# Kernel optimization log

Hardware: AMD Instinct MI355X
Metric: run time of the kernel (lower is better)

## Reference

```python
import jax, jax.numpy as jnp
import numpy as np
from jax import lax

LATENT_DIM = 512
TOKEN_DIM = 256
KERNEL = 5
STRIDE = 5


def setup_inputs() -> dict:
    key = jax.random.key(0)
    ks = jax.random.split(key, 8)
    B, L, S = 8, 1024, 10240
    s = lambda fan_in: 1.0 / np.sqrt(fan_in)
    return {
        "latents": jax.random.normal(ks[0], (B, L, LATENT_DIM), dtype=jnp.float32),
        "tokens": jax.random.normal(ks[1], (B, S, TOKEN_DIM), dtype=jnp.float32),
        # nn.Linear weights, stored as (out, in) like torch
        "W_lat": jax.random.uniform(ks[2], (LATENT_DIM, LATENT_DIM), jnp.float32, -s(LATENT_DIM), s(LATENT_DIM)),
        "W_tok": jax.random.uniform(ks[3], (LATENT_DIM, LATENT_DIM), jnp.float32, -s(LATENT_DIM), s(LATENT_DIM)),
        "W_vlat": jax.random.uniform(ks[4], (LATENT_DIM, LATENT_DIM), jnp.float32, -s(LATENT_DIM), s(LATENT_DIM)),
        "W_vtok": jax.random.uniform(ks[5], (LATENT_DIM, LATENT_DIM), jnp.float32, -s(LATENT_DIM), s(LATENT_DIM)),
        # Conv1d weight (out_ch, in_ch, k) and bias
        "conv_w": jax.random.uniform(ks[6], (LATENT_DIM, TOKEN_DIM, KERNEL), jnp.float32, -s(TOKEN_DIM * KERNEL), s(TOKEN_DIM * KERNEL)),
        "conv_b": jax.random.uniform(ks[7], (LATENT_DIM,), jnp.float32, -s(TOKEN_DIM * KERNEL), s(TOKEN_DIM * KERNEL)),
    }


def reference(latents, tokens, W_lat, W_tok, W_vlat, W_vtok, conv_w, conv_b):
    # Conv1d: (B,S,token_dim) -> (B,S//5,latent_dim)
    tok = lax.conv_general_dilated(
        tokens.transpose(0, 2, 1), conv_w, window_strides=(STRIDE,),
        padding="VALID", dimension_numbers=("NCH", "OIH", "NCH"))
    tok = (tok + conv_b[None, :, None]).transpose(0, 2, 1)  # (B, S', D)

    R_lat = jnp.einsum("bld,ed->ble", latents, W_lat)
    R_tok = jnp.einsum("bsd,ed->bse", tok, W_tok)
    V_lat = jnp.einsum("bld,ed->ble", latents, W_vlat)
    V_tok = jnp.einsum("bsd,ed->bse", tok, W_vtok)

    # shared score matrix, used for both row-wise and column-wise softmax
    A = jnp.einsum("ble,bse->bls", R_lat, R_tok) / jnp.sqrt(jnp.float32(LATENT_DIM))
    delta_lat = jnp.einsum("bls,bse->ble", jax.nn.softmax(A, axis=-1), V_tok)
    delta_tok = jnp.einsum("bls,ble->bse", jax.nn.softmax(A, axis=1), V_lat)

    updated_latents = latents + delta_lat
    updated_tokens = tok + delta_tok
    output = jnp.concatenate([updated_latents, updated_tokens], axis=1)
    return (updated_latents, updated_tokens, output)
```

## Files before the change

### kernel.cpp

```cpp
#include <hip/hip_runtime.h>
#include <math.h>

#define SCALEF 0.044194173824159216f

typedef __attribute__((ext_vector_type(8))) short bf16x8;
typedef __attribute__((ext_vector_type(4))) float f32x4;

static __device__ __forceinline__ unsigned short f2bf(float f) {
    union { float f; unsigned int i; } v; v.f = f;
    return (unsigned short)((v.i + 0x7fffu + ((v.i >> 16) & 1u)) >> 16);
}
static __device__ __forceinline__ float bf2f(unsigned short h) {
    union { unsigned int i; float f; } v; v.i = ((unsigned int)h) << 16;
    return v.f;
}
static __device__ __forceinline__ void gload16(const void* g, void* l) {
    __builtin_amdgcn_global_load_lds(
        (const __attribute__((address_space(1))) unsigned int*)g,
        (__attribute__((address_space(3))) unsigned int*)l, 16, 0, 0);
}

__global__ __launch_bounds__(256) void cvt_tl(const float4* __restrict__ tok,
                                              const float4* __restrict__ lat,
                                              ushort4* __restrict__ tokd,
                                              ushort4* __restrict__ latd) {
    long t = blockIdx.x * 256L + threadIdx.x;
    #pragma unroll
    for (int k = 0; k < 5; ++k) {
        long i = t + k * 1048576L;
        float4 f = tok[i];
        ushort4 u; u.x = f2bf(f.x); u.y = f2bf(f.y); u.z = f2bf(f.z); u.w = f2bf(f.w);
        tokd[i] = u;
    }
    {
        float4 f = lat[t];
        ushort4 u; u.x = f2bf(f.x); u.y = f2bf(f.y); u.z = f2bf(f.z); u.w = f2bf(f.w);
        latd[t] = u;
    }
}

__global__ __launch_bounds__(256) void prep_rest(
    const float4* __restrict__ wl, const float4* __restrict__ wt,
    const float4* __restrict__ wvl, const float4* __restrict__ wvt,
    const float* __restrict__ cw,
    ushort4* __restrict__ wlb, ushort4* __restrict__ wtb,
    ushort4* __restrict__ wvlb, ushort4* __restrict__ wvtb,
    unsigned int* __restrict__ wpb)
{
    const long NW = 65536, NCV = 327680;
    for (long i = blockIdx.x * 256L + threadIdx.x; i < 4 * NW + NCV;
         i += gridDim.x * 256L) {
        long r = i;
        const float4* s = nullptr; ushort4* d = nullptr;
        if (r < NW) { s = wl; d = wlb; }
        else if ((r -= NW) < NW) { s = wt; d = wtb; }
        else if ((r -= NW) < NW) { s = wvl; d = wvlb; }
        else if ((r -= NW) < NW) { s = wvt; d = wvtb; }
        else {
            r -= NW;
            long e = r / 640, rr = r % 640, k = rr >> 7, c2 = rr & 127;
            unsigned int lo = f2bf(cw[e * 1280 + (2 * c2) * 5 + k]);
            unsigned int hi = f2bf(cw[e * 1280 + (2 * c2 + 1) * 5 + k]);
            wpb[r] = lo | (hi << 16);
            continue;
        }
        float4 f = s[r];
        ushort4 u; u.x = f2bf(f.x); u.y = f2bf(f.y); u.z = f2bf(f.z); u.w = f2bf(f.w);
        d[r] = u;
    }
}

__global__ __launch_bounds__(256) void transpose_bf(const unsigned short* __restrict__ S,
                                                    unsigned short* __restrict__ ST) {
    __shared__ unsigned short tl[64][66];
    const int b = blockIdx.z, r0 = blockIdx.y << 6, c0 = blockIdx.x << 6;
    const unsigned short* Sb = S + ((long)b << 21);
    unsigned short* Tb = ST + ((long)b << 21);
    const int t32 = threadIdx.x & 31, trow = threadIdx.x >> 5;
    #pragma unroll
    for (int i = 0; i < 8; ++i) {
        int r = trow + i * 8;
        unsigned int v = *(const unsigned int*)&Sb[(long)(r0 + r) * 2048 + c0 + t32 * 2];
        *(unsigned int*)&tl[r][t32 * 2] = v;
    }
    __syncthreads();
    #pragma unroll
    for (int i = 0; i < 8; ++i) {
        int c = trow + i * 8;
        unsigned int lo = tl[t32 * 2][c], hi = tl[t32 * 2 + 1][c];
        *(unsigned int*)&Tb[(long)(c0 + c) * 1024 + r0 + t32 * 2] = lo | (hi << 16);
    }
}

template<int RL>
static __device__ __forceinline__ void sm_body(unsigned short* __restrict__ rowp,
                                               float* __restrict__ redm,
                                               float* __restrict__ reds) {
    constexpr int U = RL / 512;
    unsigned int* p = (unsigned int*)rowp;
    const int t = threadIdx.x, lane = t & 63, wid = t >> 6;
    unsigned int u[U];
    float v[2 * U];
    #pragma unroll
    for (int i = 0; i < U; ++i) u[i] = p[t + (i << 8)];
    #pragma unroll
    for (int i = 0; i < U; ++i) {
        v[2 * i]     = bf2f((unsigned short)(u[i] & 0xffffu));
        v[2 * i + 1] = bf2f((unsigned short)(u[i] >> 16));
    }
    float m = -INFINITY;
    #pragma unroll
    for (int i = 0; i < 2 * U; ++i) m = fmaxf(m, v[i]);
    #pragma unroll
    for (int k = 1; k < 64; k <<= 1) m = fmaxf(m, __shfl_xor(m, k));
    if (lane == 0) redm[wid] = m;
    __syncthreads();
    m = fmaxf(fmaxf(redm[0], redm[1]), fmaxf(redm[2], redm[3]));
    float s = 0.f, e[2 * U];
    #pragma unroll
    for (int i = 0; i < 2 * U; ++i) { e[i] = __expf(v[i] - m); s += e[i]; }
    #pragma unroll
    for (int k = 1; k < 64; k <<= 1) s += __shfl_xor(s, k);
    if (lane == 0) reds[wid] = s;
    __syncthreads();
    s = reds[0] + reds[1] + reds[2] + reds[3];
    float inv = 1.f / s;
    #pragma unroll
    for (int i = 0; i < U; ++i) {
        unsigned int lo = f2bf(e[2 * i] * inv);
        unsigned int hi = f2bf(e[2 * i + 1] * inv);
        p[t + (i << 8)] = lo | (hi << 16);
    }
}

__global__ __launch_bounds__(256) void softmax_both(unsigned short* __restrict__ S,
                                                    unsigned short* __restrict__ ST) {
    __shared__ float redm[4], reds[4];
    long b = blockIdx.x;
    if (b < 8192) sm_body<2048>(S + b * 2048L, redm, reds);
    else          sm_body<1024>(ST + (b - 8192) * 1024L, redm, reds);
}

template<int AMODE, int EPI>
static __device__ __forceinline__ void mm_body(
    char* __restrict__ smc, int bx, int by, int z,
    const unsigned short* __restrict__ A, const unsigned short* __restrict__ B,
    long bsA, long bsB, int lda, int ldb, int K,
    unsigned short* __restrict__ Cb, long bsCb,
    float* __restrict__ C0, long bsC0, float* __restrict__ C1, long bsC1,
    const void* __restrict__ basep, long bsBase, int ldc, float scale)
{
    const int t = threadIdx.x, lane = t & 63, wid = t >> 6;
    const int m0 = by << 7, n0 = bx << 7;
    const unsigned short* Ab = A + (long)z * bsA;
    const unsigned short* Bb = B + (long)z * bsB;

    const int rA0 = wid * 16 + (lane >> 2);
    const int rA1 = rA0 + 64;
    const int cs0 = (lane & 3) ^ ((rA0 >> 1) & 3);
    const int cs1 = (lane & 3) ^ ((rA1 >> 1) & 3);

    long aoff0, aoff1;
    if (AMODE == 0) {
        aoff0 = (long)(m0 + rA0) * lda + cs0 * 8;
        aoff1 = (long)(m0 + rA1) * lda + cs1 * 8;
    } else {
        int ma = m0 + rA0, mb = m0 + rA1;
        aoff0 = (long)(ma >> 11) * 2621440 + (long)(ma & 2047) * 1280 + cs0 * 8;
        aoff1 = (long)(mb >> 11) * 2621440 + (long)(mb & 2047) * 1280 + cs1 * 8;
    }
    const long boff0 = (long)(n0 + rA0) * ldb + cs0 * 8;
    const long boff1 = (long)(n0 + rA1) * ldb + cs1 * 8;

    const int dA0 = (wid << 10), dA1 = ((wid + 4) << 10);
    const int dB0 = 8192 + (wid << 10), dB1 = 8192 + ((wid + 4) << 10);

    const int wr = wid >> 1, wc = wid & 1;
    const int l15 = lane & 15, cslot = lane >> 4;
    int offA[4], offB[4];
    #pragma unroll
    for (int i = 0; i < 4; ++i) {
        int r = wr * 64 + i * 16 + l15;
        offA[i] = r * 64 + ((cslot ^ ((r >> 1) & 3)) << 4);
        int rb = wc * 64 + i * 16 + l15;
        offB[i] = 8192 + rb * 64 + ((cslot ^ ((rb >> 1) & 3)) << 4);
    }

    f32x4 acc[4][4];
    #pragma unroll
    for (int i = 0; i < 4; ++i)
        #pragma unroll
        for (int j = 0; j < 4; ++j)
            acc[i][j] = (f32x4)(0.f);

#define STAGE(p, ktv) do {                                   \
        int kb_ = (ktv);                                     \
        int bo_ = (p) * 16384;                               \
        gload16(Ab + aoff0 + kb_, smc + bo_ + dA0);          \
        gload16(Ab + aoff1 + kb_, smc + bo_ + dA1);          \
        gload16(Bb + boff0 + kb_, smc + bo_ + dB0);          \
        gload16(Bb + boff1 + kb_, smc + bo_ + dB1);          \
    } while (0)

    const int nt = K >> 5;
    STAGE(0, 0);
    STAGE(1, 32);
    int cur = 0;
    for (int it = 0; it < nt; ++it) {
        if (it + 2 < nt) {
            int nx2 = (cur >= 1) ? cur - 1 : 2;
            STAGE(nx2, (it + 2) << 5);
            asm volatile("s_waitcnt vmcnt(8)" ::: "memory");
        } else if (it + 1 < nt) {
            asm volatile("s_waitcnt vmcnt(4)" ::: "memory");
        } else {
            asm volatile("s_waitcnt vmcnt(0)" ::: "memory");
        }
        __builtin_amdgcn_s_barrier();
        const char* base = smc + cur * 16384;
        bf16x8 af[4], bfr[4];
        #pragma unroll
        for (int i = 0; i < 4; ++i) af[i]  = *(const bf16x8*)(base + offA[i]);
        #pragma unroll
        for (int i = 0; i < 4; ++i) bfr[i] = *(const bf16x8*)(base + offB[i]);
        #pragma unroll
        for (int i = 0; i < 4; ++i)
            #pragma unroll
            for (int j = 0; j < 4; ++j)
                acc[i][j] = __builtin_amdgcn_mfma_f32_16x16x32_bf16(af[i], bfr[j], acc[i][j], 0, 0, 0);
        asm volatile("s_waitcnt lgkmcnt(0)" ::: "memory");
        __builtin_amdgcn_s_barrier();
        cur = (cur + 1 == 3) ? 0 : cur + 1;
    }
#undef STAGE

    const int colb = n0 + wc * 64 + l15;
    const int rowb = m0 + wr * 64 + cslot * 4;
    #pragma unroll
    for (int i = 0; i < 4; ++i) {
        #pragma unroll
        for (int j = 0; j < 4; ++j) {
            int n = colb + j * 16;
            #pragma unroll
            for (int q = 0; q < 4; ++q) {
                int m = rowb + i * 16 + q;
                float v = acc[i][j][q];
                if (EPI == 0) {
                    Cb[(long)z * bsCb + (long)m * ldc + n] = f2bf(v * scale);
                } else if (EPI == 1) {
                    v += ((const float*)basep)[n];
                    Cb[(long)m * ldc + n] = f2bf(v);
                } else if (EPI == 2) {
                    float bv = ((const float*)basep)[(long)z * bsBase + (long)m * ldc + n];
                    float o = bv + v;
                    C0[(long)z * bsC0 + (long)m * ldc + n] = o;
                    C1[(long)z * bsC1 + (long)m * ldc + n] = o;
                } else {
                    float bv = bf2f(((const unsigned short*)basep)[(long)z * bsBase + (long)m * ldc + n]);
                    float o = bv + v;
                    C0[(long)z * bsC0 + (long)m * ldc + n] = o;
                    C1[(long)z * bsC1 + (long)m * ldc + n] = o;
                }
            }
        }
    }
}

template<int AMODE, int EPI>
__global__ __launch_bounds__(256) void mm_nt(
    const unsigned short* __restrict__ A, const unsigned short* __restrict__ B,
    long bsA, long bsB, int lda, int ldb, int K,
    unsigned short* __restrict__ Cb, long bsCb,
    float* __restrict__ C0, long bsC0, float* __restrict__ C1, long bsC1,
    const void* __restrict__ basep, long bsBase, int ldc, float scale)
{
    __shared__ unsigned short sm[24576];
    mm_body<AMODE, EPI>((char*)sm, blockIdx.x, blockIdx.y, blockIdx.z,
                        A, B, bsA, bsB, lda, ldb, K, Cb, bsCb,
                        C0, bsC0, C1, bsC1, basep, bsBase, ldc, scale);
}

__global__ __launch_bounds__(256) void gemm_g1(
    const unsigned short* __restrict__ tknb, const unsigned short* __restrict__ wpb,
    const float* __restrict__ conv_b, unsigned short* __restrict__ tokb,
    const unsigned short* __restrict__ latb, const unsigned short* __restrict__ wlb,
    unsigned short* __restrict__ rlat,
    const unsigned short* __restrict__ wvlb, unsigned short* __restrict__ vlT)
{
    __shared__ unsigned short sm[24576];
    char* smc = (char*)sm;
    const int bid = blockIdx.x;
    if (bid < 512) {
        int l = bid;
        mm_body<1, 1>(smc, l & 3, l >> 2, 0, tknb, wpb, 0, 0, 1280, 1280, 1280,
                      tokb, 0, nullptr, 0, nullptr, 0, conv_b, 0, 512, 1.f);
    } else if (bid < 768) {
        int l = bid - 512;
        mm_body<0, 0>(smc, l & 3, l >> 2, 0, latb, wlb, 0, 0, 512, 512, 512,
                      rlat, 0, nullptr, 0, nullptr, 0, nullptr, 0, 512, 1.f);
    } else {
        int l = bid - 768;
        mm_body<0, 0>(smc, l & 7, (l >> 3) & 3, l >> 5, wvlb, latb, 0, 524288,
                      512, 512, 512, vlT, 524288, nullptr, 0, nullptr, 0,
                      nullptr, 0, 1024, 1.f);
    }
}

__global__ __launch_bounds__(256) void gemm_g2(
    const unsigned short* __restrict__ tokb, const unsigned short* __restrict__ wtb,
    unsigned short* __restrict__ rtok,
    const unsigned short* __restrict__ wvtb, unsigned short* __restrict__ vtT)
{
    __shared__ unsigned short sm[24576];
    char* smc = (char*)sm;
    const int bid = blockIdx.x;
    if (bid < 512) {
        int l = bid;
        mm_body<0, 0>(smc, l & 3, l >> 2, 0, tokb, wtb, 0, 0, 512, 512, 512,
                      rtok, 0, nullptr, 0, nullptr, 0, nullptr, 0, 512, 1.f);
    } else {
        int l = bid - 512;
        mm_body<0, 0>(smc, l & 15, (l >> 4) & 3, l >> 6, wvtb, tokb, 0, 1048576,
                      512, 512, 512, vtT, 1048576, nullptr, 0, nullptr, 0,
                      nullptr, 0, 2048, 1.f);
    }
}

__global__ __launch_bounds__(256) void gemm_g3(
    const unsigned short* __restrict__ S, const unsigned short* __restrict__ ST,
    const unsigned short* __restrict__ vlT, const unsigned short* __restrict__ vtT,
    const float* __restrict__ latents, const unsigned short* __restrict__ tokb,
    float* __restrict__ out)
{
    __shared__ unsigned short sm[24576];
    char* smc = (char*)sm;
    const int bid = blockIdx.x;
    if (bid < 256) {
        int l = bid;
        mm_body<0, 2>(smc, l & 3, (l >> 2) & 7, l >> 5, S, vtT, 2097152, 1048576,
                      2048, 2048, 2048, nullptr, 0,
                      out, 524288, out + 12582912, 1572864,
                      latents, 524288, 512, 1.f);
    } else {
        int l = bid - 256;
        mm_body<0, 3>(smc, l & 3, (l >> 2) & 15, l >> 6, ST, vlT, 2097152, 524288,
                      1024, 1024, 1024, nullptr, 0,
                      out + 4194304, 1048576, out + 12582912 + 524288, 1572864,
                      tokb, 1048576, 512, 1.f);
    }
}

extern "C" void kernel_launch(void* const* d_in, const int* in_sizes, int n_in,
                              void* d_out, int out_size, void* d_ws, size_t ws_size,
                              hipStream_t stream)
{
    const float* latents = (const float*)d_in[0];
    const float* tokens  = (const float*)d_in[1];
    const float* W_lat   = (const float*)d_in[2];
    const float* W_tok   = (const float*)d_in[3];
    const float* W_vlat  = (const float*)d_in[4];
    const float* W_vtok  = (const float*)d_in[5];
    const float* conv_w  = (const float*)d_in[6];
    const float* conv_b  = (const float*)d_in[7];
    float* out = (float*)d_out;
    char* ws = (char*)d_ws;

    unsigned short* S    = (unsigned short*)(ws);
    unsigned short* ST   = (unsigned short*)(ws + 33554432);
    unsigned short* tokb = (unsigned short*)(ws + 67108864);
    unsigned short* latb = (unsigned short*)(ws + 83886080);
    unsigned short* rlat = (unsigned short*)(ws + 92274688);
    unsigned short* rtok = (unsigned short*)(ws + 100663296);
    unsigned short* vlT  = (unsigned short*)(ws + 117440512);
    unsigned short* vtT  = (unsigned short*)(ws + 125829120);
    unsigned short* wpb  = (unsigned short*)(ws + 142606336);
    unsigned short* wlb  = (unsigned short*)(ws + 143917056);
    unsigned short* wtb  = (unsigned short*)(ws + 144441344);
    unsigned short* wvlb = (unsigned short*)(ws + 144965632);
    unsigned short* wvtb = (unsigned short*)(ws + 145489920);
    unsigned short* tknb = (unsigned short*)(out + 12582912);

    cvt_tl<<<4096, 256, 0, stream>>>((const float4*)tokens, (const float4*)latents,
                                     (ushort4*)tknb, (ushort4*)latb);
    prep_rest<<<512, 256, 0, stream>>>(
        (const float4*)W_lat, (const float4*)W_tok,
        (const float4*)W_vlat, (const float4*)W_vtok, conv_w,
        (ushort4*)wlb, (ushort4*)wtb, (ushort4*)wvlb, (ushort4*)wvtb,
        (unsigned int*)wpb);

    gemm_g1<<<1024, 256, 0, stream>>>(tknb, wpb, conv_b, tokb,
                                      latb, wlb, rlat, wvlb, vlT);

    gemm_g2<<<1024, 256, 0, stream>>>(tokb, wtb, rtok, wvtb, vtT);

    mm_nt<0, 0><<<dim3(16, 8, 8), 256, 0, stream>>>(
        rlat, rtok, 524288, 1048576, 512, 512, 512, S, 2097152,
        nullptr, 0, nullptr, 0, nullptr, 0, 2048, SCALEF);
    transpose_bf<<<dim3(32, 16, 8), 256, 0, stream>>>(S, ST);

    softmax_both<<<24576, 256, 0, stream>>>(S, ST);

    gemm_g3<<<768, 256, 0, stream>>>(S, ST, vlT, vtT, latents, tokb, out);
}
```

Baseline: 244.7 us.

## Fuse score transpose into score GEMM epilogue and swizzle block order for XCDs

The score GEMM now writes both S and its transpose ST directly from its epilogue, with 4-row ushort4 stores into ST. This removes the separate transpose kernel, its launch and the extra read and write of S. Block indices in all grouped GEMM kernels are remapped with a swizzle that spreads consecutive blocks across the 8 XCDs. This is meant to improve L2 locality. The row stores into S are now scalar 2-byte writes strided by ldc, which may hurt coalescing of the S writes.

```diff
diff --git a/kernel.cpp b/kernel.cpp
--- a/kernel.cpp
+++ b/kernel.cpp
@@ -18,6 +18,9 @@
     __builtin_amdgcn_global_load_lds(
         (const __attribute__((address_space(1))) unsigned int*)g,
         (__attribute__((address_space(3))) unsigned int*)l, 16, 0, 0);
+}
+static __device__ __forceinline__ int swz(int l, int n) {
+    return (l & 7) * (n >> 3) + (l >> 3);
 }
 
 __global__ __launch_bounds__(256) void cvt_tl(const float4* __restrict__ tok,
@@ -70,28 +73,6 @@
     }
 }
 
-__global__ __launch_bounds__(256) void transpose_bf(const unsigned short* __restrict__ S,
-                                                    unsigned short* __restrict__ ST) {
-    __shared__ unsigned short tl[64][66];
-    const int b = blockIdx.z, r0 = blockIdx.y << 6, c0 = blockIdx.x << 6;
-    const unsigned short* Sb = S + ((long)b << 21);
-    unsigned short* Tb = ST + ((long)b << 21);
-    const int t32 = threadIdx.x & 31, trow = threadIdx.x >> 5;
-    #pragma unroll
-    for (int i = 0; i < 8; ++i) {
-        int r = trow + i * 8;
-        unsigned int v = *(const unsigned int*)&Sb[(long)(r0 + r) * 2048 + c0 + t32 * 2];
-        *(unsigned int*)&tl[r][t32 * 2] = v;
-    }
-    __syncthreads();
-    #pragma unroll
-    for (int i = 0; i < 8; ++i) {
-        int c = trow + i * 8;
-        unsigned int lo = tl[t32 * 2][c], hi = tl[t32 * 2 + 1][c];
-        *(unsigned int*)&Tb[(long)(c0 + c) * 1024 + r0 + t32 * 2] = lo | (hi << 16);
-    }
-}
-
 template<int RL>
 static __device__ __forceinline__ void sm_body(unsigned short* __restrict__ rowp,
                                                float* __restrict__ redm,
@@ -236,6 +217,25 @@
 
     const int colb = n0 + wc * 64 + l15;
     const int rowb = m0 + wr * 64 + cslot * 4;
+    if (EPI == 4) {
+        unsigned short* STp = (unsigned short*)C0;
+        #pragma unroll
+        for (int i = 0; i < 4; ++i) {
+            #pragma unroll
+            for (int j = 0; j < 4; ++j) {
+                int n = colb + j * 16;
+                int mb = rowb + i * 16;
+                float v0 = acc[i][j][0] * scale, v1 = acc[i][j][1] * scale;
+                float v2 = acc[i][j][2] * scale, v3 = acc[i][j][3] * scale;
+                unsigned short b0 = f2bf(v0), b1 = f2bf(v1), b2 = f2bf(v2), b3 = f2bf(v3);
+                unsigned short* sp = Cb + (long)z * bsCb + (long)mb * ldc + n;
+                sp[0] = b0; sp[ldc] = b1; sp[2 * ldc] = b2; sp[3 * ldc] = b3;
+                ushort4 st4; st4.x = b0; st4.y = b1; st4.z = b2; st4.w = b3;
+                *(ushort4*)(STp + (long)z * bsC0 + (long)n * bsC1 + mb) = st4;
+            }
+        }
+        return;
+    }
     #pragma unroll
     for (int i = 0; i < 4; ++i) {
         #pragma unroll
@@ -266,20 +266,6 @@
     }
 }
 
-template<int AMODE, int EPI>
-__global__ __launch_bounds__(256) void mm_nt(
-    const unsigned short* __restrict__ A, const unsigned short* __restrict__ B,
-    long bsA, long bsB, int lda, int ldb, int K,
-    unsigned short* __restrict__ Cb, long bsCb,
-    float* __restrict__ C0, long bsC0, float* __restrict__ C1, long bsC1,
-    const void* __restrict__ basep, long bsBase, int ldc, float scale)
-{
-    __shared__ unsigned short sm[24576];
-    mm_body<AMODE, EPI>((char*)sm, blockIdx.x, blockIdx.y, blockIdx.z,
-                        A, B, bsA, bsB, lda, ldb, K, Cb, bsCb,
-                        C0, bsC0, C1, bsC1, basep, bsBase, ldc, scale);
-}
-
 __global__ __launch_bounds__(256) void gemm_g1(
     const unsigned short* __restrict__ tknb, const unsigned short* __restrict__ wpb,
     const float* __restrict__ conv_b, unsigned short* __restrict__ tokb,
@@ -291,15 +277,15 @@
     char* smc = (char*)sm;
     const int bid = blockIdx.x;
     if (bid < 512) {
-        int l = bid;
+        int l = swz(bid, 512);
         mm_body<1, 1>(smc, l & 3, l >> 2, 0, tknb, wpb, 0, 0, 1280, 1280, 1280,
                       tokb, 0, nullptr, 0, nullptr, 0, conv_b, 0, 512, 1.f);
     } else if (bid < 768) {
-        int l = bid - 512;
+        int l = swz(bid - 512, 256);
         mm_body<0, 0>(smc, l & 3, l >> 2, 0, latb, wlb, 0, 0, 512, 512, 512,
                       rlat, 0, nullptr, 0, nullptr, 0, nullptr, 0, 512, 1.f);
     } else {
-        int l = bid - 768;
+        int l = swz(bid - 768, 256);
         mm_body<0, 0>(smc, l & 7, (l >> 3) & 3, l >> 5, wvlb, latb, 0, 524288,
                       512, 512, 512, vlT, 524288, nullptr, 0, nullptr, 0,
                       nullptr, 0, 1024, 1.f);
@@ -315,15 +301,27 @@
     char* smc = (char*)sm;
     const int bid = blockIdx.x;
     if (bid < 512) {
-        int l = bid;
+        int l = swz(bid, 512);
         mm_body<0, 0>(smc, l & 3, l >> 2, 0, tokb, wtb, 0, 0, 512, 512, 512,
                       rtok, 0, nullptr, 0, nullptr, 0, nullptr, 0, 512, 1.f);
     } else {
-        int l = bid - 512;
+        int l = swz(bid - 512, 512);
         mm_body<0, 0>(smc, l & 15, (l >> 4) & 3, l >> 6, wvtb, tokb, 0, 1048576,
                       512, 512, 512, vtT, 1048576, nullptr, 0, nullptr, 0,
                       nullptr, 0, 2048, 1.f);
     }
+}
+
+__global__ __launch_bounds__(256) void gemm_sc(
+    const unsigned short* __restrict__ rlat, const unsigned short* __restrict__ rtok,
+    unsigned short* __restrict__ S, unsigned short* __restrict__ ST)
+{
+    __shared__ unsigned short sm[24576];
+    int l = swz((int)blockIdx.x, 1024);
+    mm_body<0, 4>((char*)sm, l & 15, (l >> 4) & 7, l >> 7,
+                  rlat, rtok, 524288, 1048576, 512, 512, 512,
+                  S, 2097152, (float*)ST, 2097152, nullptr, 1024,
+                  nullptr, 0, 2048, SCALEF);
 }
 
 __global__ __launch_bounds__(256) void gemm_g3(
@@ -336,13 +334,13 @@
     char* smc = (char*)sm;
     const int bid = blockIdx.x;
     if (bid < 256) {
-        int l = bid;
+        int l = swz(bid, 256);
         mm_body<0, 2>(smc, l & 3, (l >> 2) & 7, l >> 5, S, vtT, 2097152, 1048576,
                       2048, 2048, 2048, nullptr, 0,
                       out, 524288, out + 12582912, 1572864,
                       latents, 524288, 512, 1.f);
     } else {
-        int l = bid - 256;
+        int l = swz(bid - 256, 512);
         mm_body<0, 3>(smc, l & 3, (l >> 2) & 15, l >> 6, ST, vlT, 2097152, 524288,
                       1024, 1024, 1024, nullptr, 0,
                       out + 4194304, 1048576, out + 12582912 + 524288, 1572864,
@@ -393,10 +391,7 @@
 
     gemm_g2<<<1024, 256, 0, stream>>>(tokb, wtb, rtok, wvtb, vtT);
 
-    mm_nt<0, 0><<<dim3(16, 8, 8), 256, 0, stream>>>(
-        rlat, rtok, 524288, 1048576, 512, 512, 512, S, 2097152,
-        nullptr, 0, nullptr, 0, nullptr, 0, 2048, SCALEF);
-    transpose_bf<<<dim3(32, 16, 8), 256, 0, stream>>>(S, ST);
+    gemm_sc<<<1024, 256, 0, stream>>>(rlat, rtok, S, ST);
 
     softmax_both<<<24576, 256, 0, stream>>>(S, ST);
 
```

Measured after the change: 226.6 us. 7.4% less time.
